# Optimization experiments

Measured on AMD Instinct MI355X. Metric: run time of the kernel, lower is better.

## Reference

```python
import jax, jax.numpy as jnp
import numpy as np

N_NODES = 50000
N_EDGES = 800000
NUM_FEATURES = 128
HIDDEN = 128
NUM_CLASSES = 10
NUM_GRAPHS = 512
PROCESSING_STEPS = 4


def setup_inputs() -> dict:
    key = jax.random.key(0)
    ks = jax.random.split(key, 20)
    s = 0.05
    inp = {
        'x': jax.random.normal(ks[0], (N_NODES, NUM_FEATURES), jnp.float32),
        'edge_index': jax.random.randint(ks[1], (2, N_EDGES), 0, N_NODES),
        'batch': jnp.sort(jax.random.randint(ks[2], (N_NODES,), 0, NUM_GRAPHS)),
        # GCN layers (weights stored [in, out])
        'W1': jax.random.normal(ks[3], (NUM_FEATURES, HIDDEN), jnp.float32) * s,
        'b1': jnp.zeros((HIDDEN,), jnp.float32),
        'W2': jax.random.normal(ks[4], (HIDDEN, HIDDEN), jnp.float32) * s,
        'b2': jnp.zeros((HIDDEN,), jnp.float32),
        'W3': jax.random.normal(ks[5], (HIDDEN, HIDDEN), jnp.float32) * s,
        'b3': jnp.zeros((HIDDEN,), jnp.float32),
        # Set2Set LSTM cell: input 2*HIDDEN -> hidden HIDDEN, torch gate order i,f,g,o
        'Wih': jax.random.normal(ks[6], (4 * HIDDEN, 2 * HIDDEN), jnp.float32) * s,
        'Whh': jax.random.normal(ks[7], (4 * HIDDEN, HIDDEN), jnp.float32) * s,
        'bih': jnp.zeros((4 * HIDDEN,), jnp.float32),
        'bhh': jnp.zeros((4 * HIDDEN,), jnp.float32),
        # MLP head
        'L1w': jax.random.normal(ks[8], (2 * HIDDEN, HIDDEN), jnp.float32) * s,
        'L1b': jnp.zeros((HIDDEN,), jnp.float32),
        'L2w': jax.random.normal(ks[9], (HIDDEN, HIDDEN // 2), jnp.float32) * s,
        'L2b': jnp.zeros((HIDDEN // 2,), jnp.float32),
        'L3w': jax.random.normal(ks[10], (HIDDEN // 2, NUM_CLASSES), jnp.float32) * s,
        'L3b': jnp.zeros((NUM_CLASSES,), jnp.float32),
    }
    return inp


def _gcn_conv(x, row, col, W, b, n):
    # PyG GCNConv: x @ W, symmetric normalization with self-loops, scatter-add to targets.
    xw = x @ W  # [N, out]
    deg = jax.ops.segment_sum(jnp.ones_like(col, dtype=xw.dtype), col, num_segments=n)
    dis = jnp.where(deg > 0, jax.lax.rsqrt(jnp.maximum(deg, 1.0)), 0.0)
    norm = dis[row] * dis[col]  # [E+N]
    out = jax.ops.segment_sum(norm[:, None] * xw[row], col, num_segments=n)
    return out + b


def _segment_softmax(e, batch, n_seg):
    emax = jax.lax.stop_gradient(jax.ops.segment_max(e, batch, num_segments=n_seg))
    emax = jnp.where(jnp.isfinite(emax), emax, 0.0)
    a = jnp.exp(e - emax[batch])
    asum = jax.ops.segment_sum(a, batch, num_segments=n_seg)
    return a / jnp.where(asum > 0, asum, 1.0)[batch]


def reference(x, edge_index, batch, W1, b1, W2, b2, W3, b3,
              Wih, Whh, bih, bhh, L1w, L1b, L2w, L2b, L3w, L3b):
    n = x.shape[0]
    # add self loops once
    loops = jnp.arange(n, dtype=edge_index.dtype)
    row = jnp.concatenate([edge_index[0], loops])  # sources
    col = jnp.concatenate([edge_index[1], loops])  # targets

    h = jax.nn.relu(_gcn_conv(x, row, col, W1, b1, n))
    h = jax.nn.relu(_gcn_conv(h, row, col, W2, b2, n))
    h = jax.nn.relu(_gcn_conv(h, row, col, W3, b3, n))

    # Set2Set readout (processing_steps=4)
    d = h.shape[1]
    hs = jnp.zeros((NUM_GRAPHS, d), h.dtype)
    cs = jnp.zeros((NUM_GRAPHS, d), h.dtype)
    q_star = jnp.zeros((NUM_GRAPHS, 2 * d), h.dtype)
    for _ in range(PROCESSING_STEPS):
        gates = q_star @ Wih.T + hs @ Whh.T + bih + bhh  # [B, 4d]
        ig, fg, gg, og = jnp.split(gates, 4, axis=-1)
        cs = jax.nn.sigmoid(fg) * cs + jax.nn.sigmoid(ig) * jnp.tanh(gg)
        q = jax.nn.sigmoid(og) * jnp.tanh(cs)
        hs = q
        e = jnp.sum(h * q[batch], axis=-1)  # [N]
        a = _segment_softmax(e, batch, NUM_GRAPHS)
        r = jax.ops.segment_sum(a[:, None] * h, batch, num_segments=NUM_GRAPHS)
        q_star = jnp.concatenate([q, r], axis=-1)

    # MLP head (dropout inactive in eval)
    y = jax.nn.relu(q_star @ L1w + L1b)
    y = jax.nn.relu(y @ L2w + L2b)
    y = y @ L3w + L3b
    return jax.nn.log_softmax(y, axis=-1)
```

## Files before the change

### kernel.cpp

```cpp
#include <hip/hip_runtime.h>

constexpr int NN  = 50000;
constexpr int NE  = 800000;
constexpr int FD  = 128;
constexpr int NG  = 512;
constexpr int NB  = 4;
constexpr int BCAP = 24;
constexpr int CAP = NB * BCAP;
constexpr int SLICE = 12500;
constexpr int NBKT   = 196;
constexpr int BNODES = 256;
constexpr int CAPB   = 6144;

typedef __attribute__((ext_vector_type(8))) short bf16x8;
typedef __attribute__((ext_vector_type(4))) float f32x4;

__device__ __forceinline__ float bf2f(unsigned short u) {
    unsigned int v = ((unsigned int)u) << 16;
    float f; __builtin_memcpy(&f, &v, 4); return f;
}
__device__ __forceinline__ unsigned short f2bf(float f) {
    unsigned int u; __builtin_memcpy(&u, &f, 4);
    u += 0x7FFFu + ((u >> 16) & 1u);
    return (unsigned short)(u >> 16);
}
__device__ __forceinline__ float2 bfp(unsigned int u) {
    unsigned int lo = u << 16, hi = u & 0xFFFF0000u;
    float2 r; __builtin_memcpy(&r.x, &lo, 4); __builtin_memcpy(&r.y, &hi, 4);
    return r;
}
__device__ __forceinline__ unsigned int packbf(float a, float b) {
    return (unsigned int)f2bf(a) | ((unsigned int)f2bf(b) << 16);
}
__device__ __forceinline__ float sigmoidf(float x) { return 1.0f / (1.0f + __expf(-x)); }
__device__ __forceinline__ float ldw(const void* p, int idx, int flag) {
    return flag ? ((const float*)p)[idx] : bf2f(((const unsigned short*)p)[idx]);
}

__global__ void k_detect(const unsigned int* __restrict__ xw, int* __restrict__ flag,
                         int* __restrict__ gcnt) {
    if (threadIdx.x < NBKT) gcnt[threadIdx.x] = 0;
    __shared__ int cnt;
    if (threadIdx.x == 0) cnt = 0;
    __syncthreads();
    int local = 0;
    for (int i = threadIdx.x; i < 2048; i += 256) {
        unsigned int w = xw[i];
        unsigned int h0 = w & 0xFFFFu, h1 = w >> 16;
        if (((h0 >> 7) & 0xFF) >= 0x90) local++;
        if (((h1 >> 7) & 0xFF) >= 0x90) local++;
    }
    atomicAdd(&cnt, local);
    __syncthreads();
    if (threadIdx.x == 0) *flag = (cnt > 256) ? 1 : 0;
}

__global__ void k_cvt_x(const void* __restrict__ src, unsigned short* __restrict__ dst,
                        const int* __restrict__ batch, int* __restrict__ goff,
                        const int* __restrict__ flagp) {
    int i = blockIdx.x * 256 + threadIdx.x;
    if (i < NN * FD / 8) {
        if (*flagp) {
            const float4* s = (const float4*)src;
            float4 a = s[2 * i], b = s[2 * i + 1];
            uint4 o;
            o.x = packbf(a.x, a.y); o.y = packbf(a.z, a.w);
            o.z = packbf(b.x, b.y); o.w = packbf(b.z, b.w);
            ((uint4*)dst)[i] = o;
        } else {
            ((uint4*)dst)[i] = ((const uint4*)src)[i];
        }
    }
    if (i < NN) {
        int b = batch[i];
        if (b < 0) b = 0;
        if (b >= NG) b = NG - 1;
        int prev;
        if (i == 0) prev = -1;
        else {
            prev = batch[i - 1];
            if (prev < 0) prev = 0;
            if (prev >= NG) prev = NG - 1;
        }
        for (int g = prev + 1; g <= b; g++) goff[g] = i;
        if (i == NN - 1)
            for (int g = b + 1; g <= NG; g++) goff[g] = NN;
    }
}

struct WDesc {
    const void* src[12];
    void* dst[12];
    int kind[12];
    int off[13];
};
__global__ void k_cvt_w(WDesc d, const int* __restrict__ flagp) {
    int gid = blockIdx.x * 256 + threadIdx.x;
    if (gid >= d.off[12]) return;
    int flag = *flagp;
    int t = 0;
    while (gid >= d.off[t + 1]) t++;
    int i = gid - d.off[t];
    if (d.kind[t] == 0) {
        if (flag) ((unsigned short*)d.dst[t])[i] = f2bf(((const float*)d.src[t])[i]);
        else      ((unsigned short*)d.dst[t])[i] = ((const unsigned short*)d.src[t])[i];
    } else {
        int n = i >> 6, k2 = i & 63;
        ((unsigned int*)d.dst[t])[i] = packbf(ldw(d.src[t], (2 * k2) * 128 + n, flag),
                                              ldw(d.src[t], (2 * k2 + 1) * 128 + n, flag));
    }
}

__global__ void k_wt(const void* __restrict__ Wih, const void* __restrict__ Whh,
                     const void* __restrict__ bih, const void* __restrict__ bhh,
                     unsigned int* __restrict__ WcombT,
                     unsigned int* __restrict__ WrT,
                     float* __restrict__ bsum, const int* __restrict__ flagp) {
    int gid = blockIdx.x * 256 + threadIdx.x;
    int flag = *flagp;
    if (gid < 64 * 512) {
        int k2 = gid >> 9, row = gid & 511;
        float a0 = ldw(Wih, row * 256 + 2 * k2, flag)     + ldw(Whh, row * 128 + 2 * k2, flag);
        float a1 = ldw(Wih, row * 256 + 2 * k2 + 1, flag) + ldw(Whh, row * 128 + 2 * k2 + 1, flag);
        WcombT[(k2 >> 1) * 1024 + 2 * row + (k2 & 1)] = packbf(a0, a1);
    } else if (gid < 2 * 64 * 512) {
        int g2 = gid - 64 * 512;
        int k2 = g2 >> 9, row = g2 & 511;
        WrT[(k2 >> 1) * 1024 + 2 * row + (k2 & 1)] =
            packbf(ldw(Wih, row * 256 + 128 + 2 * k2, flag),
                   ldw(Wih, row * 256 + 128 + 2 * k2 + 1, flag));
    } else if (gid < 2 * 64 * 512 + 512) {
        int row = gid - 2 * 64 * 512;
        bsum[row] = ldw(bih, row, flag) + ldw(bhh, row, flag);
    }
}

__global__ __launch_bounds__(256) void k_fill1(const int* __restrict__ ei,
                                               int* __restrict__ gcnt,
                                               unsigned int* __restrict__ bktbuf) {
    __shared__ int hist[NBKT];
    __shared__ int wbase[NBKT];
    int t = threadIdx.x;
    for (int i = t; i < NBKT; i += 256) hist[i] = 0;
    __syncthreads();
    int base_e = blockIdx.x * 2048;
    int bb[8], rk[8];
    unsigned int pk[8];
#pragma unroll
    for (int k = 0; k < 8; k++) {
        int e = base_e + k * 256 + t;
        if (e < NE) {
            int r = ei[e], c = ei[NE + e];
            if ((unsigned)r >= (unsigned)NN) r = 0;
            if ((unsigned)c >= (unsigned)NN) c = 0;
            bb[k] = c >> 8;
            rk[k] = atomicAdd(&hist[bb[k]], 1);
            pk[k] = ((unsigned)c << 16) | (unsigned)r;
        } else bb[k] = -1;
    }
    __syncthreads();
    for (int i = t; i < NBKT; i += 256)
        wbase[i] = hist[i] ? atomicAdd(&gcnt[i], hist[i]) : 0;
    __syncthreads();
#pragma unroll
    for (int k = 0; k < 8; k++) {
        if (bb[k] >= 0) {
            int pos = wbase[bb[k]] + rk[k];
            if (pos < CAPB) bktbuf[bb[k] * CAPB + pos] = pk[k];
        }
    }
}

__global__ __launch_bounds__(512) void k_fill2(const unsigned int* __restrict__ bktbuf,
                                               const int* __restrict__ gcnt,
                                               int* __restrict__ bcnt,
                                               unsigned short* __restrict__ csr_row) {
    int b = blockIdx.x, t = threadIdx.x;
    __shared__ int lcnt[BNODES * NB];
    for (int i = t; i < BNODES * NB; i += 512) lcnt[i] = 0;
    uint4* creg = (uint4*)(csr_row + (size_t)b * BNODES * CAP);
    for (int i = t; i < BNODES * CAP / 8; i += 512)
        creg[i] = (uint4){0, 0, 0, 0};
    __syncthreads();
    int n = gcnt[b]; if (n > CAPB) n = CAPB;
    const unsigned int* bp = bktbuf + (size_t)b * CAPB;
    for (int i = t; i < n; i += 512) {
        unsigned int v = bp[i];
        int r = v & 0xFFFFu;
        int c = v >> 16;
        int cl = c & (BNODES - 1);
        int nb = r / SLICE;
        int pos = atomicAdd(&lcnt[cl * NB + nb], 1);
        if (pos < BCAP)
            csr_row[(size_t)c * CAP + nb * BCAP + pos] = (unsigned short)r;
    }
    __syncthreads();
    for (int i = t; i < BNODES * NB; i += 512) {
        int node = b * BNODES + (i >> 2);
        if (node < NN) bcnt[(size_t)node * NB + (i & 3)] = lcnt[i];
    }
}

__global__ __launch_bounds__(256) void k_gemm(const unsigned short* __restrict__ H,
                                              const unsigned int* __restrict__ WT,
                                              const int4* __restrict__ bcnt4,
                                              unsigned short* __restrict__ XW, int M) {
    __shared__ alignas(16) unsigned short WB[128 * 136];
    int t = threadIdx.x;
    unsigned int* WBu = (unsigned int*)WB;
    for (int c = t; c < 2048; c += 256) {
        uint4 v = ((const uint4*)WT)[c];
        int n = c >> 4, k2q = c & 15;
        *(uint4*)(WBu + n * 68 + k2q * 4) = v;
    }
    __syncthreads();
    int wave = t >> 6, lane = t & 63;
    int lm = lane & 15;
    int lq = lane >> 4;
    int row = blockIdx.x * 64 + wave * 16 + lm;
    int rowc = (row < M) ? row : (M - 1);
    const unsigned short* Arow = H + (size_t)rowc * 128;
    f32x4 acc[8];
#pragma unroll
    for (int n = 0; n < 8; n++) acc[n] = (f32x4){0.f, 0.f, 0.f, 0.f};
#pragma unroll
    for (int kk = 0; kk < 4; kk++) {
        bf16x8 afrag = *(const bf16x8*)(Arow + kk * 32 + lq * 8);
        const unsigned short* wbase = WB + kk * 32 + lq * 8;
#pragma unroll
        for (int n = 0; n < 8; n++) {
            bf16x8 bfrag = *(const bf16x8*)(wbase + (n * 16 + lm) * 136);
            acc[n] = __builtin_amdgcn_mfma_f32_16x16x32_bf16(afrag, bfrag, acc[n], 0, 0, 0);
        }
    }
    __syncthreads();
#pragma unroll
    for (int r = 0; r < 4; r++) {
        int row_local = wave * 16 + lq * 4 + r;
        int orow = blockIdx.x * 64 + row_local;
        int oc = (orow < M) ? orow : (M - 1);
        int4 bc = bcnt4[oc];
        float dn = rsqrtf((float)(bc.x + bc.y + bc.z + bc.w + 1));
#pragma unroll
        for (int n = 0; n < 8; n++)
            WB[row_local * 136 + n * 16 + lm] = f2bf(acc[n][r] * dn);
    }
#pragma unroll
    for (int it = 0; it < 4; it++) {
        int row_local = wave * 16 + it * 4 + (lane >> 4);
        int row_global = blockIdx.x * 64 + row_local;
        uint4 v = *(const uint4*)(WB + row_local * 136 + (lane & 15) * 8);
        if (row_global < M)
            *((uint4*)(XW + (size_t)row_global * 128) + (lane & 15)) = v;
    }
}

__global__ __launch_bounds__(256) void k_aggr(const unsigned short* __restrict__ XW,
                                              const int4* __restrict__ bcnt4,
                                              const unsigned short* __restrict__ csr_row,
                                              const unsigned short* __restrict__ bias,
                                              unsigned short* __restrict__ Hout) {
    int wave = threadIdx.x >> 6;
    int lane = threadIdx.x & 63;
    int nsel = lane >> 4;
    int sub  = lane & 15;
    int node = blockIdx.x * 16 + wave * 4 + nsel;
    if (node >= NN) return;
    const uint4* XW4 = (const uint4*)XW;
    int4 bc = bcnt4[node];
    int deg = bc.x + bc.y + bc.z + bc.w;
    float dn = rsqrtf((float)(deg + 1));
    uint4 sv = XW4[(size_t)node * 16 + sub];
    float2 s0 = bfp(sv.x), s1 = bfp(sv.y), s2 = bfp(sv.z), s3 = bfp(sv.w);
    float a0 = s0.x, a1 = s0.y, a2 = s1.x, a3 = s1.y;
    float a4 = s2.x, a5 = s2.y, a6 = s3.x, a7 = s3.y;
    int cnts[NB] = {bc.x, bc.y, bc.z, bc.w};
    const unsigned short* lst = csr_row + (size_t)node * CAP;
#pragma unroll
    for (int b = 0; b < NB; b++) {
        int n = cnts[b]; if (n > BCAP) n = BCAP;
        const unsigned short* lb = lst + b * BCAP;
        int j = 0;
        for (; j + 4 <= n; j += 4) {
            int r0 = lb[j], r1 = lb[j + 1], r2 = lb[j + 2], r3 = lb[j + 3];
            uint4 v0 = XW4[(size_t)r0 * 16 + sub];
            uint4 v1 = XW4[(size_t)r1 * 16 + sub];
            uint4 v2 = XW4[(size_t)r2 * 16 + sub];
            uint4 v3 = XW4[(size_t)r3 * 16 + sub];
            float2 f;
            f = bfp(v0.x); a0 += f.x; a1 += f.y;
            f = bfp(v0.y); a2 += f.x; a3 += f.y;
            f = bfp(v0.z); a4 += f.x; a5 += f.y;
            f = bfp(v0.w); a6 += f.x; a7 += f.y;
            f = bfp(v1.x); a0 += f.x; a1 += f.y;
            f = bfp(v1.y); a2 += f.x; a3 += f.y;
            f = bfp(v1.z); a4 += f.x; a5 += f.y;
            f = bfp(v1.w); a6 += f.x; a7 += f.y;
            f = bfp(v2.x); a0 += f.x; a1 += f.y;
            f = bfp(v2.y); a2 += f.x; a3 += f.y;
            f = bfp(v2.z); a4 += f.x; a5 += f.y;
            f = bfp(v2.w); a6 += f.x; a7 += f.y;
            f = bfp(v3.x); a0 += f.x; a1 += f.y;
            f = bfp(v3.y); a2 += f.x; a3 += f.y;
            f = bfp(v3.z); a4 += f.x; a5 += f.y;
            f = bfp(v3.w); a6 += f.x; a7 += f.y;
        }
        for (; j < n; j++) {
            int r = lb[j];
            uint4 v = XW4[(size_t)r * 16 + sub];
            float2 f;
            f = bfp(v.x); a0 += f.x; a1 += f.y;
            f = bfp(v.y); a2 += f.x; a3 += f.y;
            f = bfp(v.z); a4 += f.x; a5 += f.y;
            f = bfp(v.w); a6 += f.x; a7 += f.y;
        }
    }
    uint4 bv = ((const uint4*)bias)[sub];
    float2 b0 = bfp(bv.x), b1 = bfp(bv.y), b2 = bfp(bv.z), b3 = bfp(bv.w);
    uint4 o;
    o.x = packbf(fmaxf(dn * a0 + b0.x, 0.0f), fmaxf(dn * a1 + b0.y, 0.0f));
    o.y = packbf(fmaxf(dn * a2 + b1.x, 0.0f), fmaxf(dn * a3 + b1.y, 0.0f));
    o.z = packbf(fmaxf(dn * a4 + b2.x, 0.0f), fmaxf(dn * a5 + b2.y, 0.0f));
    o.w = packbf(fmaxf(dn * a6 + b3.x, 0.0f), fmaxf(dn * a7 + b3.y, 0.0f));
    ((uint4*)Hout)[(size_t)node * 16 + sub] = o;
}

__global__ __launch_bounds__(512) void k_s2s(const unsigned short* __restrict__ H,
                                             const int* __restrict__ goff,
                                             const unsigned int* __restrict__ WcombT,
                                             const unsigned int* __restrict__ WrT,
                                             const float* __restrict__ bsum,
                                             const unsigned short* __restrict__ L1w,
                                             const unsigned short* __restrict__ L1b,
                                             const unsigned short* __restrict__ L2w,
                                             const unsigned short* __restrict__ L2b,
                                             const unsigned short* __restrict__ L3w,
                                             const unsigned short* __restrict__ L3b,
                                             void* __restrict__ out,
                                             const int* __restrict__ flagp) {
    int g = blockIdx.x, t = threadIdx.x;
    __shared__ float qsr[256];
    __shared__ float hsv[128], csv[128];
    __shared__ float gates[512];
    __shared__ float wred[8];
    __shared__ float wrr[8][128];
    __shared__ float ps[128];
    __shared__ float qrep[4 * 132];
    __shared__ float y1[128], y2[64], y3[10], lseS[1];

    if (t < 256) qsr[t] = 0.0f;
    if (t < 128) { hsv[t] = 0.0f; csv[t] = 0.0f; }
    __syncthreads();

    int s = goff[g], e = goff[g + 1];
    if (s < 0) s = 0;
    if (e > NN) e = NN;
    if (e < s) e = s;
    int w = t >> 6, lane = t & 63;
    const unsigned int* Hu = (const unsigned int*)H;

    int nq = t >> 2;
    int fq = (t & 3) * 16;
    const float* qc = qrep + (t & 3) * 132 + 2 * fq;
    const uint2* WC2 = (const uint2*)WcombT;
    const uint2* WR2 = (const uint2*)WrT;

    for (int step = 0; step < 4; step++) {
        {
            float accA = bsum[t], accB = 0.0f, accC = 0.0f, accD = 0.0f;
#pragma unroll 8
            for (int p = 0; p < 32; p++) {
                uint2 u = WC2[p * 512 + t];
                float2 w0 = bfp(u.x), w1 = bfp(u.y);
                accA += w0.x * hsv[4 * p];     accB += w0.y * hsv[4 * p + 1];
                accC += w1.x * hsv[4 * p + 2]; accD += w1.y * hsv[4 * p + 3];
            }
#pragma unroll 8
            for (int p = 0; p < 32; p++) {
                uint2 u = WR2[p * 512 + t];
                float2 w0 = bfp(u.x), w1 = bfp(u.y);
                accA += w0.x * qsr[128 + 4 * p];     accB += w0.y * qsr[128 + 4 * p + 1];
                accC += w1.x * qsr[128 + 4 * p + 2]; accD += w1.y * qsr[128 + 4 * p + 3];
            }
            gates[t] = (accA + accB) + (accC + accD);
        }
        __syncthreads();
        if (t < 128) {
            float ig = sigmoidf(gates[t]),       fg = sigmoidf(gates[128 + t]);
            float gg = tanhf(gates[256 + t]),    og = sigmoidf(gates[384 + t]);
            float c = fg * csv[t] + ig * gg;
            float q = og * tanhf(c);
            csv[t] = c;
            hsv[t] = q;
            qsr[t] = q;
            qrep[t] = q; qrep[132 + t] = q; qrep[264 + t] = q; qrep[396 + t] = q;
        }
        __syncthreads();

        float m = -1e30f, l = 0.0f, r0 = 0.0f, r1 = 0.0f;
        for (int cs = s; cs < e; cs += 128) {
            int ce = cs + 128; if (ce > e) ce = e;
            int nid = cs + nq;
            float eacc = 0.0f;
            if (nid < ce) {
                const unsigned int* hrow = Hu + (size_t)nid * 64 + fq;
#pragma unroll
                for (int u = 0; u < 16; u += 4) {
                    uint4 hv = *(const uint4*)(hrow + u);
                    float2 f0 = bfp(hv.x), f1 = bfp(hv.y);
                    float2 f2 = bfp(hv.z), f3 = bfp(hv.w);
                    const float* qp = qc + 2 * u;
                    eacc += f0.x * qp[0] + f0.y * qp[1] + f1.x * qp[2] + f1.y * qp[3]
                          + f2.x * qp[4] + f2.y * qp[5] + f3.x * qp[6] + f3.y * qp[7];
                }
            }
            eacc += __shfl_xor(eacc, 1);
            eacc += __shfl_xor(eacc, 2);
            float esc = (nid < ce) ? eacc : -1e30f;
            float vmax = esc;
            for (int d = 4; d < 64; d <<= 1) vmax = fmaxf(vmax, __shfl_xor(vmax, d));
            if (lane == 0) wred[w] = vmax;
            __syncthreads();
            float M = m;
#pragma unroll
            for (int k = 0; k < 8; k++) M = fmaxf(M, wred[k]);
            float p = __expf(esc - M);
            bool lead = ((t & 3) == 0) && (nid < ce);
            if (lead) ps[nq] = p;
            float psum = lead ? p : 0.0f;
            for (int d = 1; d < 64; d <<= 1) psum += __shfl_xor(psum, d);
            __syncthreads();
            if (lane == 0) wred[w] = psum;
            __syncthreads();
            float Lc = 0.0f;
#pragma unroll
            for (int k = 0; k < 8; k++) Lc += wred[k];
            float scale = __expf(m - M);
            l = l * scale + Lc;
            r0 *= scale; r1 *= scale;
            m = M;
            int i = cs + w;
            for (; i + 24 < ce; i += 32) {
                float p0 = ps[i - cs],      p1 = ps[i + 8 - cs];
                float p2 = ps[i + 16 - cs], p3 = ps[i + 24 - cs];
                unsigned int v0 = Hu[(size_t)i * 64 + lane];
                unsigned int v1 = Hu[(size_t)(i + 8) * 64 + lane];
                unsigned int v2 = Hu[(size_t)(i + 16) * 64 + lane];
                unsigned int v3 = Hu[(size_t)(i + 24) * 64 + lane];
                float2 f0 = bfp(v0), f1 = bfp(v1), f2 = bfp(v2), f3 = bfp(v3);
                r0 += p0 * f0.x + p1 * f1.x + p2 * f2.x + p3 * f3.x;
                r1 += p0 * f0.y + p1 * f1.y + p2 * f2.y + p3 * f3.y;
            }
            for (; i < ce; i += 8) {
                float p0 = ps[i - cs];
                float2 f = bfp(Hu[(size_t)i * 64 + lane]);
                r0 += p0 * f.x; r1 += p0 * f.y;
            }
            __syncthreads();
        }
        wrr[w][2 * lane]     = r0;
        wrr[w][2 * lane + 1] = r1;
        __syncthreads();
        if (t < 128) {
            float R = 0.0f;
#pragma unroll
            for (int k = 0; k < 8; k++) R += wrr[k][t];
            float L = l;
            if (!(L > 0.0f)) L = 1.0f;
            qsr[128 + t] = R / L;
        }
        __syncthreads();
    }

    if (t < 128) {
        float acc = bf2f(L1b[t]);
        for (int i = 0; i < 256; i++) acc += bf2f(L1w[i * 128 + t]) * qsr[i];
        y1[t] = fmaxf(acc, 0.0f);
    }
    __syncthreads();
    if (t < 64) {
        float a2 = bf2f(L2b[t]);
        for (int i = 0; i < 128; i++) a2 += bf2f(L2w[i * 64 + t]) * y1[i];
        y2[t] = fmaxf(a2, 0.0f);
    }
    __syncthreads();
    if (t < 10) {
        float a3 = bf2f(L3b[t]);
        for (int i = 0; i < 64; i++) a3 += bf2f(L3w[i * 10 + t]) * y2[i];
        y3[t] = a3;
    }
    __syncthreads();
    if (t == 0) {
        float m = y3[0];
        for (int i = 1; i < 10; i++) m = fmaxf(m, y3[i]);
        float s2 = 0.0f;
        for (int i = 0; i < 10; i++) s2 += __expf(y3[i] - m);
        lseS[0] = m + __logf(s2);
    }
    __syncthreads();
    if (t < 10) {
        float v = y3[t] - lseS[0];
        if (!(v == v)) v = -9.0f;
        if (*flagp) ((float*)out)[g * 10 + t] = v;
        else        ((unsigned short*)out)[g * 10 + t] = f2bf(v);
    }
}

extern "C" void kernel_launch(void* const* d_in, const int* in_sizes, int n_in,
                              void* d_out, int out_size, void* d_ws, size_t ws_size,
                              hipStream_t stream) {
    const int* ei  = (const int*)d_in[1];
    const int* bat = (const int*)d_in[2];

    char* base = (char*)d_ws;
    size_t woff = 0;
    auto alloc = [&](size_t bytes) -> void* {
        void* r = base + woff;
        woff = (woff + bytes + 255) & ~(size_t)255;
        return r;
    };
    unsigned short* A = (unsigned short*)alloc((size_t)NN * FD * 2);
    unsigned short* B = (unsigned short*)alloc((size_t)NN * FD * 2);
    unsigned short* csr_row = (unsigned short*)alloc((size_t)NBKT * BNODES * CAP * 2);
    int*   bcnt     = (int*)alloc((size_t)NN * NB * 4);
    int*   goff     = (int*)alloc((NG + 1) * 4);
    int*   flag     = (int*)alloc(256);
    int*   gcnt     = (int*)alloc(NBKT * 4);
    unsigned int* WcombT = (unsigned int*)alloc(64 * 512 * 4);
    unsigned int* WrT    = (unsigned int*)alloc(64 * 512 * 4);
    float* bsum          = (float*)alloc(512 * 4);
    unsigned int* cWT1 = (unsigned int*)alloc(8192 * 4);
    unsigned int* cWT2 = (unsigned int*)alloc(8192 * 4);
    unsigned int* cWT3 = (unsigned int*)alloc(8192 * 4);
    auto walloc = [&](int n) { return (unsigned short*)alloc((size_t)n * 2); };
    unsigned short* cb1  = walloc(128);
    unsigned short* cb2  = walloc(128);
    unsigned short* cb3  = walloc(128);
    unsigned short* cL1w = walloc(256 * 128);
    unsigned short* cL1b = walloc(128);
    unsigned short* cL2w = walloc(128 * 64);
    unsigned short* cL2b = walloc(64);
    unsigned short* cL3w = walloc(64 * 10);
    unsigned short* cL3b = walloc(10);
    unsigned int* bktbuf = (unsigned int*)A;
    (void)ws_size; (void)in_sizes; (void)n_in; (void)out_size;

    k_detect<<<1, 256, 0, stream>>>((const unsigned int*)d_in[0], flag, gcnt);
    k_cvt_x<<<(NN * FD / 8 + 255) / 256, 256, 0, stream>>>(d_in[0], B, bat, goff, flag);
    {
        WDesc d;
        const int idxs[12]  = {3,    4,  5,    6,  7,    8,  13, 14, 15, 16, 17, 18};
        void* dsts[12]      = {cWT1, cb1, cWT2, cb2, cWT3, cb3,
                               cL1w, cL1b, cL2w, cL2b, cL3w, cL3b};
        const int kinds[12] = {1, 0, 1, 0, 1, 0, 0, 0, 0, 0, 0, 0};
        const int ns[12]    = {8192, 128, 8192, 128, 8192, 128,
                               256 * 128, 128, 128 * 64, 64, 64 * 10, 10};
        int acc = 0;
        for (int i = 0; i < 12; i++) {
            d.src[i] = d_in[idxs[i]];
            d.dst[i] = dsts[i];
            d.kind[i] = kinds[i];
            d.off[i] = acc;
            acc += ns[i];
        }
        d.off[12] = acc;
        k_cvt_w<<<(acc + 255) / 256, 256, 0, stream>>>(d, flag);
    }
    k_wt<<<(2 * 64 * 512 + 512 + 255) / 256, 256, 0, stream>>>(
        d_in[9], d_in[10], d_in[11], d_in[12], WcombT, WrT, bsum, flag);

    k_fill1<<<(NE + 2047) / 2048, 256, 0, stream>>>(ei, gcnt, bktbuf);
    k_fill2<<<NBKT, 512, 0, stream>>>(bktbuf, gcnt, bcnt, csr_row);

    const int gemmBlk = (NN + 63) / 64;
    const int aggrBlk = (NN + 15) / 16;

    k_gemm<<<gemmBlk, 256, 0, stream>>>(B, cWT1, (const int4*)bcnt, A, NN);
    k_aggr<<<aggrBlk, 256, 0, stream>>>(A, (const int4*)bcnt, csr_row, cb1, B);
    k_gemm<<<gemmBlk, 256, 0, stream>>>(B, cWT2, (const int4*)bcnt, A, NN);
    k_aggr<<<aggrBlk, 256, 0, stream>>>(A, (const int4*)bcnt, csr_row, cb2, B);
    k_gemm<<<gemmBlk, 256, 0, stream>>>(B, cWT3, (const int4*)bcnt, A, NN);
    k_aggr<<<aggrBlk, 256, 0, stream>>>(A, (const int4*)bcnt, csr_row, cb3, B);

    k_s2s<<<NG, 512, 0, stream>>>(B, goff, WcombT, WrT, bsum,
                                  cL1w, cL1b, cL2w, cL2b, cL3w, cL3b,
                                  d_out, flag);
}
```

Measured before the change: 319.9 us.

## Double Set2Set block to 1024 threads, splitting gate GEMV and node work

The Set2Set readout kernel now runs 1024 threads per graph instead of 512. The LSTM gate GEMV is split in half along the reduction dimension, with partial sums combined in shared memory. Node attention uses 8 threads per node instead of 4, and the weighted readout strides over 16 warps. The aim is more latency hiding and memory-level parallelism per graph, at the cost of more block-wide reductions, a larger shared footprint, and higher register pressure under the 1024 launch bound.

```diff
diff --git a/kernel.cpp b/kernel.cpp
--- a/kernel.cpp
+++ b/kernel.cpp
@@ -325,7 +325,7 @@
     ((uint4*)Hout)[(size_t)node * 16 + sub] = o;
 }
 
-__global__ __launch_bounds__(512) void k_s2s(const unsigned short* __restrict__ H,
+__global__ __launch_bounds__(1024) void k_s2s(const unsigned short* __restrict__ H,
                                              const int* __restrict__ goff,
                                              const unsigned int* __restrict__ WcombT,
                                              const unsigned int* __restrict__ WrT,
@@ -341,11 +341,11 @@
     int g = blockIdx.x, t = threadIdx.x;
     __shared__ float qsr[256];
     __shared__ float hsv[128], csv[128];
-    __shared__ float gates[512];
-    __shared__ float wred[8];
-    __shared__ float wrr[8][128];
+    __shared__ float pg[1024];
+    __shared__ float wred[16];
+    __shared__ float wrr[16][128];
     __shared__ float ps[128];
-    __shared__ float qrep[4 * 132];
+    __shared__ float qrep[8 * 132];
     __shared__ float y1[128], y2[64], y3[10], lseS[1];
 
     if (t < 256) qsr[t] = 0.0f;
@@ -359,41 +359,46 @@
     int w = t >> 6, lane = t & 63;
     const unsigned int* Hu = (const unsigned int*)H;
 
-    int nq = t >> 2;
-    int fq = (t & 3) * 16;
-    const float* qc = qrep + (t & 3) * 132 + 2 * fq;
+    int gate = t & 511, hf = t >> 9;
+    int p0 = hf * 16;
+    int nq = t >> 3;
+    int fq = (t & 7) * 8;
+    const float* qc = qrep + (t & 7) * 132 + 2 * fq;
     const uint2* WC2 = (const uint2*)WcombT;
     const uint2* WR2 = (const uint2*)WrT;
 
     for (int step = 0; step < 4; step++) {
         {
-            float accA = bsum[t], accB = 0.0f, accC = 0.0f, accD = 0.0f;
+            float accA = 0.0f, accB = 0.0f, accC = 0.0f, accD = 0.0f;
 #pragma unroll 8
-            for (int p = 0; p < 32; p++) {
-                uint2 u = WC2[p * 512 + t];
+            for (int p = p0; p < p0 + 16; p++) {
+                uint2 u = WC2[p * 512 + gate];
                 float2 w0 = bfp(u.x), w1 = bfp(u.y);
                 accA += w0.x * hsv[4 * p];     accB += w0.y * hsv[4 * p + 1];
                 accC += w1.x * hsv[4 * p + 2]; accD += w1.y * hsv[4 * p + 3];
             }
 #pragma unroll 8
-            for (int p = 0; p < 32; p++) {
-                uint2 u = WR2[p * 512 + t];
+            for (int p = p0; p < p0 + 16; p++) {
+                uint2 u = WR2[p * 512 + gate];
                 float2 w0 = bfp(u.x), w1 = bfp(u.y);
                 accA += w0.x * qsr[128 + 4 * p];     accB += w0.y * qsr[128 + 4 * p + 1];
                 accC += w1.x * qsr[128 + 4 * p + 2]; accD += w1.y * qsr[128 + 4 * p + 3];
             }
-            gates[t] = (accA + accB) + (accC + accD);
+            pg[hf * 512 + gate] = (accA + accB) + (accC + accD);
         }
         __syncthreads();
         if (t < 128) {
-            float ig = sigmoidf(gates[t]),       fg = sigmoidf(gates[128 + t]);
-            float gg = tanhf(gates[256 + t]),    og = sigmoidf(gates[384 + t]);
+            float ig = sigmoidf(bsum[t]       + pg[t]       + pg[512 + t]);
+            float fg = sigmoidf(bsum[128 + t] + pg[128 + t] + pg[640 + t]);
+            float gg = tanhf(   bsum[256 + t] + pg[256 + t] + pg[768 + t]);
+            float og = sigmoidf(bsum[384 + t] + pg[384 + t] + pg[896 + t]);
             float c = fg * csv[t] + ig * gg;
             float q = og * tanhf(c);
             csv[t] = c;
             hsv[t] = q;
             qsr[t] = q;
-            qrep[t] = q; qrep[132 + t] = q; qrep[264 + t] = q; qrep[396 + t] = q;
+#pragma unroll
+            for (int rp = 0; rp < 8; rp++) qrep[rp * 132 + t] = q;
         }
         __syncthreads();
 
@@ -405,7 +410,7 @@
             if (nid < ce) {
                 const unsigned int* hrow = Hu + (size_t)nid * 64 + fq;
 #pragma unroll
-                for (int u = 0; u < 16; u += 4) {
+                for (int u = 0; u < 8; u += 4) {
                     uint4 hv = *(const uint4*)(hrow + u);
                     float2 f0 = bfp(hv.x), f1 = bfp(hv.y);
                     float2 f2 = bfp(hv.z), f3 = bfp(hv.w);
@@ -416,16 +421,17 @@
             }
             eacc += __shfl_xor(eacc, 1);
             eacc += __shfl_xor(eacc, 2);
+            eacc += __shfl_xor(eacc, 4);
             float esc = (nid < ce) ? eacc : -1e30f;
             float vmax = esc;
-            for (int d = 4; d < 64; d <<= 1) vmax = fmaxf(vmax, __shfl_xor(vmax, d));
+            for (int d = 8; d < 64; d <<= 1) vmax = fmaxf(vmax, __shfl_xor(vmax, d));
             if (lane == 0) wred[w] = vmax;
             __syncthreads();
             float M = m;
 #pragma unroll
-            for (int k = 0; k < 8; k++) M = fmaxf(M, wred[k]);
+            for (int k = 0; k < 16; k++) M = fmaxf(M, wred[k]);
             float p = __expf(esc - M);
-            bool lead = ((t & 3) == 0) && (nid < ce);
+            bool lead = ((t & 7) == 0) && (nid < ce);
             if (lead) ps[nq] = p;
             float psum = lead ? p : 0.0f;
             for (int d = 1; d < 64; d <<= 1) psum += __shfl_xor(psum, d);
@@ -434,27 +440,27 @@
             __syncthreads();
             float Lc = 0.0f;
 #pragma unroll
-            for (int k = 0; k < 8; k++) Lc += wred[k];
+            for (int k = 0; k < 16; k++) Lc += wred[k];
             float scale = __expf(m - M);
             l = l * scale + Lc;
             r0 *= scale; r1 *= scale;
             m = M;
             int i = cs + w;
-            for (; i + 24 < ce; i += 32) {
-                float p0 = ps[i - cs],      p1 = ps[i + 8 - cs];
-                float p2 = ps[i + 16 - cs], p3 = ps[i + 24 - cs];
+            for (; i + 48 < ce; i += 64) {
+                float p0_ = ps[i - cs],      p1_ = ps[i + 16 - cs];
+                float p2_ = ps[i + 32 - cs], p3_ = ps[i + 48 - cs];
                 unsigned int v0 = Hu[(size_t)i * 64 + lane];
-                unsigned int v1 = Hu[(size_t)(i + 8) * 64 + lane];
-                unsigned int v2 = Hu[(size_t)(i + 16) * 64 + lane];
-                unsigned int v3 = Hu[(size_t)(i + 24) * 64 + lane];
+                unsigned int v1 = Hu[(size_t)(i + 16) * 64 + lane];
+                unsigned int v2 = Hu[(size_t)(i + 32) * 64 + lane];
+                unsigned int v3 = Hu[(size_t)(i + 48) * 64 + lane];
                 float2 f0 = bfp(v0), f1 = bfp(v1), f2 = bfp(v2), f3 = bfp(v3);
-                r0 += p0 * f0.x + p1 * f1.x + p2 * f2.x + p3 * f3.x;
-                r1 += p0 * f0.y + p1 * f1.y + p2 * f2.y + p3 * f3.y;
+                r0 += p0_ * f0.x + p1_ * f1.x + p2_ * f2.x + p3_ * f3.x;
+                r1 += p0_ * f0.y + p1_ * f1.y + p2_ * f2.y + p3_ * f3.y;
             }
-            for (; i < ce; i += 8) {
-                float p0 = ps[i - cs];
+            for (; i < ce; i += 16) {
+                float p0_ = ps[i - cs];
                 float2 f = bfp(Hu[(size_t)i * 64 + lane]);
-                r0 += p0 * f.x; r1 += p0 * f.y;
+                r0 += p0_ * f.x; r1 += p0_ * f.y;
             }
             __syncthreads();
         }
@@ -464,7 +470,7 @@
         if (t < 128) {
             float R = 0.0f;
 #pragma unroll
-            for (int k = 0; k < 8; k++) R += wrr[k][t];
+            for (int k = 0; k < 16; k++) R += wrr[k][t];
             float L = l;
             if (!(L > 0.0f)) L = 1.0f;
             qsr[128 + t] = R / L;
@@ -582,7 +588,7 @@
     k_gemm<<<gemmBlk, 256, 0, stream>>>(B, cWT3, (const int4*)bcnt, A, NN);
     k_aggr<<<aggrBlk, 256, 0, stream>>>(A, (const int4*)bcnt, csr_row, cb3, B);
 
-    k_s2s<<<NG, 512, 0, stream>>>(B, goff, WcombT, WrT, bsum,
-                                  cL1w, cL1b, cL2w, cL2b, cL3w, cL3b,
-                                  d_out, flag);
-}
+    k_s2s<<<NG, 1024, 0, stream>>>(B, goff, WcombT, WrT, bsum,
+                                   cL1w, cL1b, cL2w, cL2b, cL3w, cL3b,
+                                   d_out, flag);
+}
```

Result: slower. 350.2 us (+9.5%).
